# Kernel optimization log

Hardware: AMD Instinct MI355X
Metric: run time of the kernel (lower is better)

The kernel has to match this reference:

```python
import jax, jax.numpy as jnp
import numpy as np

BN_EPS = 1e-5


def setup_inputs() -> dict:
    key = jax.random.key(0)
    ks = jax.random.split(key, 8)
    B, C, H, W = 8, 256, 48, 48
    s = 1.0 / np.sqrt(C)
    x = jax.random.normal(ks[0], (B, C, H, W), dtype=jnp.float32)
    Wk = jax.random.normal(ks[1], (C, C), dtype=jnp.float32) * s
    Wq = jax.random.normal(ks[2], (C, C), dtype=jnp.float32) * s
    Wv = jax.random.normal(ks[3], (C, C), dtype=jnp.float32) * s
    W2 = jax.random.normal(ks[4], (C, C), dtype=jnp.float32) * s
    b2 = jax.random.normal(ks[5], (C,), dtype=jnp.float32) * 0.02
    gamma = jnp.ones((C,), dtype=jnp.float32)
    beta = jnp.zeros((C,), dtype=jnp.float32)
    return {"x": x, "Wk": Wk, "Wq": Wq, "Wv": Wv, "W2": W2, "b2": b2,
            "gamma": gamma, "beta": beta}


def reference(x, Wk, Wq, Wv, W2, b2, gamma, beta):
    B, C, H, W = x.shape
    N = H * W
    xf = x.reshape(B, C, N)
    # 1x1 convs == channel mixing matmuls
    k = jnp.einsum('oc,bcn->bon', Wk, xf)  # (B,C,N)
    q = jnp.einsum('oc,bcn->bon', Wq, xf)  # (B,C,N)
    v = jnp.einsum('oc,bcn->bon', Wv, xf)  # (B,C,N)
    # scores[b,n,m] = sum_c k[b,c,n] * q[b,c,m]  (unscaled, as in source)
    scores = jnp.einsum('bcn,bcm->bnm', k, q)          # (B,N,N)
    prob = jax.nn.softmax(scores, axis=2)
    # out[b,c,n] = sum_m prob[b,n,m] * v[b,c,m]
    attn = jnp.einsum('bnm,bcm->bcn', prob, v).reshape(B, C, H, W)
    # react2: 1x1 conv (with bias) + BatchNorm2d (training-mode batch stats)
    y = jnp.einsum('oc,bchw->bohw', W2, attn) + b2[None, :, None, None]
    mean = jnp.mean(y, axis=(0, 2, 3))
    var = jnp.var(y, axis=(0, 2, 3))  # biased, matches torch BN normalization
    yhat = (y - mean[None, :, None, None]) * jax.lax.rsqrt(var + BN_EPS)[None, :, None, None]
    return yhat * gamma[None, :, None, None] + beta[None, :, None, None]
```

## Files before the change

kernel.cpp:

```cpp
#include <hip/hip_runtime.h>
#include <hip/hip_fp16.h>
#include <math.h>

#define BN_EPS 1e-5f

typedef unsigned short ushort_t;
typedef unsigned int uint_t;

constexpr int BB   = 8;
constexpr int CC   = 256;
constexpr int NN   = 2304;
constexpr int MTOT = BB * NN;
constexpr int NSPLIT = 4;
constexpr int MT32 = 72;
constexpr int TPS  = 18;
constexpr int TILE = 8192;
constexpr float MFIX = 64.0f;
constexpr size_t SZE = (size_t)BB * NN * CC;

typedef short bf16x8 __attribute__((ext_vector_type(8)));
typedef _Float16 f16x8 __attribute__((ext_vector_type(8)));
typedef float f32x16 __attribute__((ext_vector_type(16)));

union F4 { float4 v; float f[4]; };
union US4 { ushort_t u[4]; uint2 v; };
union U4H8 { uint4 v; ushort_t h[8]; };

__device__ __forceinline__ ushort_t f2bf(float f) {
  uint_t u = __float_as_uint(f);
  uint_t r = u + 0x7FFFu + ((u >> 16) & 1u);
  return (ushort_t)(r >> 16);
}
__device__ __forceinline__ float bf2f(ushort_t h) {
  return __uint_as_float(((uint_t)h) << 16);
}
__device__ __forceinline__ ushort_t f2h(float f) {
  return __half_as_ushort(__float2half(f));
}
__device__ __forceinline__ uint_t pk_trunc(float lo, float hi) {
  return __builtin_amdgcn_perm(__float_as_uint(hi), __float_as_uint(lo), 0x07060302u);
}
__device__ __forceinline__ int rowmap(int reg, int laneHi) {
  return (reg & 3) + 8 * (reg >> 2) + 4 * laneHi;
}

__global__ __launch_bounds__(256) void xpose(
    const float* __restrict__ x, ushort_t* __restrict__ xh, ushort_t* __restrict__ xl)
{
  const int b = blockIdx.z, n0 = blockIdx.y * 64, c0 = blockIdx.x * 64;
  __shared__ float t_s[64][67];
  const int tid = threadIdx.x;
#pragma unroll
  for (int t = 0; t < 4; ++t) {
    int e4 = tid + t * 256;
    int r = e4 >> 4, c4 = e4 & 15;
    F4 v; v.v = *(const float4*)&x[((size_t)b * CC + c0 + r) * NN + n0 + c4 * 4];
#pragma unroll
    for (int k = 0; k < 4; ++k) t_s[r][c4 * 4 + k] = v.f[k];
  }
  __syncthreads();
#pragma unroll
  for (int t = 0; t < 4; ++t) {
    int e = tid + t * 256;
    int nr = e >> 4, cc = e & 15;
    US4 hv, lv;
#pragma unroll
    for (int k = 0; k < 4; ++k) {
      const float v = t_s[cc * 4 + k][nr];
      const ushort_t h = f2bf(v);
      hv.u[k] = h;
      lv.u[k] = f2bf(v - bf2f(h));
    }
    const size_t o = ((size_t)b * NN + n0 + nr) * CC + c0 + cc * 4;
    *(uint2*)&xh[o] = hv.v;
    *(uint2*)&xl[o] = lv.v;
  }
}

__global__ __launch_bounds__(256) void wsplit(
    const float* __restrict__ Wk, const float* __restrict__ Wq,
    const float* __restrict__ Wv, const float* __restrict__ W2,
    ushort_t* __restrict__ wh, ushort_t* __restrict__ wl,
    float* __restrict__ stats)
{
  if (blockIdx.x < 2) stats[blockIdx.x * 256 + threadIdx.x] = 0.f;
  const int mat = blockIdx.x >> 5;
  const int off = ((blockIdx.x & 31) * 256 + threadIdx.x) * 8;
  const float* Wm = (mat == 0) ? Wk : (mat == 1) ? Wq : (mat == 2) ? Wv : W2;
  F4 a, c;
  a.v = *(const float4*)&Wm[off];
  c.v = *(const float4*)&Wm[off + 4];
  U4H8 hv, lv;
#pragma unroll
  for (int j = 0; j < 8; ++j) {
    const float v = (j < 4) ? a.f[j] : c.f[j - 4];
    const ushort_t h = f2bf(v);
    hv.h[j] = h;
    lv.h[j] = f2bf(v - bf2f(h));
  }
  *(uint4*)&wh[mat * 65536 + off] = hv.v;
  *(uint4*)&wl[mat * 65536 + off] = lv.v;
}

__global__ __launch_bounds__(256, 3) void qkv_mfma(
    const ushort_t* __restrict__ xh, const ushort_t* __restrict__ xl,
    const ushort_t* __restrict__ wh, const ushort_t* __restrict__ wl,
    ushort_t* __restrict__ kf, ushort_t* __restrict__ qf,
    ushort_t* __restrict__ vt2)
{
  const int mb  = blockIdx.x;
  const int mat = blockIdx.y >> 1;
  const int nh  = blockIdx.y & 1;
  const int b   = blockIdx.z;
  const int tid = threadIdx.x, w = tid >> 6, lane = tid & 63;
  const int l31 = lane & 31, lH = lane >> 5;
  const int wm = w & 1, wn = w >> 1;

  __shared__ alignas(16) ushort_t smem[24576];

  const size_t xrow = ((size_t)b * NN + mb * 64 + lane) * CC;
  const int obase = nh * 128;
  const size_t wrow = (size_t)(obase + lane) * CC;
  const ushort_t* whm = wh + mat * 65536;
  const ushort_t* wlm = wl + mat * 65536;

  f32x16 accA[2], accB[2], accC[2];
#pragma unroll
  for (int i = 0; i < 2; ++i) {
    accA[i] = (f32x16){}; accB[i] = (f32x16){}; accC[i] = (f32x16){};
  }

#define STAGE(k0)                                                                   \
  {                                                                                 \
    _Pragma("unroll")                                                               \
    for (int cc = 0; cc < 2; ++cc) {                                                \
      const int ch = 2 * w + cc;                                                    \
      const size_t gx = xrow + (k0) + ch * 8;                                       \
      __builtin_amdgcn_global_load_lds(                                             \
          (const __attribute__((address_space(1))) uint_t*)(xh + gx),               \
          (__attribute__((address_space(3))) uint_t*)(smem + ch * 512), 16, 0, 0);  \
      __builtin_amdgcn_global_load_lds(                                             \
          (const __attribute__((address_space(1))) uint_t*)(xl + gx),               \
          (__attribute__((address_space(3))) uint_t*)(smem + 4096 + ch * 512),      \
          16, 0, 0);                                                                \
      _Pragma("unroll")                                                             \
      for (int h = 0; h < 2; ++h) {                                                 \
        const size_t gw = wrow + (size_t)h * 64 * CC + (k0) + ch * 8;               \
        __builtin_amdgcn_global_load_lds(                                           \
            (const __attribute__((address_space(1))) uint_t*)(whm + gw),            \
            (__attribute__((address_space(3))) uint_t*)(smem + 8192 + ch * 1024 +   \
                                                        h * 512), 16, 0, 0);        \
        __builtin_amdgcn_global_load_lds(                                           \
            (const __attribute__((address_space(1))) uint_t*)(wlm + gw),            \
            (__attribute__((address_space(3))) uint_t*)(smem + 16384 + ch * 1024 +  \
                                                        h * 512), 16, 0, 0);        \
      }                                                                             \
    }                                                                               \
  }

#pragma unroll
  for (int t = 0; t < 4; ++t) {
    if (t) __syncthreads();
    STAGE(t * 64)
    __syncthreads();
#pragma unroll
    for (int kc = 0; kc < 4; ++kc) {
      const int ch = kc * 2 + lH;
      const bf16x8 Ah = *(const bf16x8*)&smem[(ch * 64 + wm * 32 + l31) * 8];
      const bf16x8 Al = *(const bf16x8*)&smem[4096 + (ch * 64 + wm * 32 + l31) * 8];
#pragma unroll
      for (int ot = 0; ot < 2; ++ot) {
        const int oL = wn * 64 + ot * 32 + l31;
        const bf16x8 Bh = *(const bf16x8*)&smem[8192 + (ch * 128 + oL) * 8];
        const bf16x8 Bl = *(const bf16x8*)&smem[16384 + (ch * 128 + oL) * 8];
        accA[ot] = __builtin_amdgcn_mfma_f32_32x32x16_bf16(Ah, Bh, accA[ot], 0, 0, 0);
        accB[ot] = __builtin_amdgcn_mfma_f32_32x32x16_bf16(Ah, Bl, accB[ot], 0, 0, 0);
        accC[ot] = __builtin_amdgcn_mfma_f32_32x32x16_bf16(Al, Bh, accC[ot], 0, 0, 0);
      }
    }
  }
#undef STAGE
  __syncthreads();

  ushort_t* vscr = smem + w * 1280;
  const int mt = mb * 2 + wm;
  const size_t tbase = (size_t)(b * MT32 + mt) * TILE;
#pragma unroll
  for (int ot = 0; ot < 2; ++ot) {
    const int o0 = obase + wn * 64 + ot * 32;
    if (mat < 2) {
#pragma unroll
      for (int reg = 0; reg < 16; ++reg)
        vscr[rowmap(reg, lH) * 40 + l31] =
            f2h(accA[ot][reg] + accB[ot][reg] + accC[ot][reg]);
      ushort_t* ob = ((mat == 0) ? kf : qf) + tbase;
#pragma unroll
      for (int k2 = 0; k2 < 2; ++k2) {
        const int idx = k2 * 64 + lane;
        const int n = idx >> 2, coct = idx & 3;
        uint4 pk = *(const uint4*)&vscr[n * 40 + coct * 8];
        *(uint4*)&ob[(size_t)(((o0 >> 3) + coct) * 32 + n) * 8] = pk;
      }
    } else {
#pragma unroll
      for (int reg = 0; reg < 16; ++reg)
        vscr[l31 * 40 + rowmap(reg, lH)] =
            f2bf(accA[ot][reg] + accB[ot][reg] + accC[ot][reg]);
#pragma unroll
      for (int k2 = 0; k2 < 2; ++k2) {
        const int idx = k2 * 64 + lane;
        const int cl = idx >> 2, moct = idx & 3;
        uint4 pk = *(const uint4*)&vscr[cl * 40 + moct * 8];
        *(uint4*)&vt2[tbase + (size_t)(moct * 256 + o0 + cl) * 8] = pk;
      }
    }
  }
}

__global__ __launch_bounds__(256, 2) void attn_fused(
    const ushort_t* __restrict__ kf, const ushort_t* __restrict__ qf,
    const ushort_t* __restrict__ vt2,
    ushort_t* __restrict__ Opart, float* __restrict__ Ls)
{
  const int id = blockIdx.x + 18 * (blockIdx.y + 4 * blockIdx.z);
  const int xcd = id & 7, s = id >> 3;
  const int g = xcd * 4 + s / 18;
  const int n0 = (s % 18) * 128;
  const int split = g & 3, b = g >> 2;

  const int tid = threadIdx.x;
  const int w = tid >> 6, lane = tid & 63;
  const int l31 = lane & 31, lH = lane >> 5;

  __shared__ alignas(16) ushort_t sQ[2 * TILE];
  __shared__ alignas(16) ushort_t sV[2 * TILE];
  __shared__ alignas(16) ushort_t sPt[4 * 1280];
  ushort_t* Pt = sPt + w * 1280;

  const ushort_t* qtb = qf + (size_t)(b * MT32 + split * TPS) * TILE;
  const ushort_t* vtb = vt2 + (size_t)(b * MT32 + split * TPS) * TILE;

  f16x8 Kf[16];
  {
    const ushort_t* kt = kf + (size_t)(b * MT32 + (n0 >> 5) + w) * TILE;
#pragma unroll
    for (int kc = 0; kc < 16; ++kc)
      Kf[kc] = *(const f16x8*)&kt[(size_t)((kc * 2 + lH) * 32 + l31) * 8];
  }
  f32x16 O[8];
#pragma unroll
  for (int i = 0; i < 8; ++i) O[i] = (f32x16){};
  float rsum = 0.f;

#define ISSUE_TILE(tt, buf)                                                        \
  {                                                                                \
    const ushort_t* qs = qtb + (size_t)(tt) * TILE;                                \
    const ushort_t* vs = vtb + (size_t)(tt) * TILE;                                \
    ushort_t* ldq = sQ + (buf) * TILE;                                             \
    ushort_t* ldv = sV + (buf) * TILE;                                             \
    _Pragma("unroll")                                                              \
    for (int j = 0; j < 4; ++j) {                                                  \
      const int i = w * 4 + j;                                                     \
      __builtin_amdgcn_global_load_lds(                                            \
          (const __attribute__((address_space(1))) uint_t*)(qs + i * 512 + lane * 8), \
          (__attribute__((address_space(3))) uint_t*)(ldq + i * 512), 16, 0, 0);   \
      __builtin_amdgcn_global_load_lds(                                            \
          (const __attribute__((address_space(1))) uint_t*)(vs + i * 512 + lane * 8), \
          (__attribute__((address_space(3))) uint_t*)(ldv + i * 512), 16, 0, 0);   \
    }                                                                              \
  }

  ISSUE_TILE(0, 0)
  ISSUE_TILE(1, 1)
  __syncthreads();

  for (int t = 0; t < TPS; ++t) {
    const int cur = t & 1;
    const ushort_t* Qs = sQ + cur * TILE;
    const ushort_t* Vs = sV + cur * TILE;
    f32x16 acc = {};
#pragma unroll
    for (int kc = 0; kc < 16; ++kc) {
      f16x8 Aq = *(const f16x8*)&Qs[(size_t)((kc * 2 + lH) * 32 + l31) * 8];
      acc = __builtin_amdgcn_mfma_f32_32x32x16_f16(Aq, Kf[kc], acc, 0, 0, 0);
    }
#pragma unroll
    for (int j = 0; j < 4; ++j) {
      float p0 = __expf(acc[4 * j]     - MFIX);
      float p1 = __expf(acc[4 * j + 1] - MFIX);
      float p2 = __expf(acc[4 * j + 2] - MFIX);
      float p3 = __expf(acc[4 * j + 3] - MFIX);
      rsum += (p0 + p1) + (p2 + p3);
      uint2 pk;
      pk.x = pk_trunc(p0, p1);
      pk.y = pk_trunc(p2, p3);
      *(uint2*)&Pt[l31 * 40 + 8 * j + 4 * lH] = pk;
    }
#pragma unroll
    for (int ks = 0; ks < 2; ++ks) {
      bf16x8 Bp = *(const bf16x8*)&Pt[l31 * 40 + ks * 16 + lH * 8];
#pragma unroll
      for (int cg = 0; cg < 8; ++cg) {
        bf16x8 Av = *(const bf16x8*)&Vs[(size_t)((ks * 2 + lH) * 256 + cg * 32 + l31) * 8];
        O[cg] = __builtin_amdgcn_mfma_f32_32x32x16_bf16(Av, Bp, O[cg], 0, 0, 0);
      }
    }
    __syncthreads();
    if (t + 2 < TPS) ISSUE_TILE(t + 2, cur)
  }
#undef ISSUE_TILE

  ushort_t* Ob = Opart + (size_t)(split * BB + b) * CC * NN;
  const int n = n0 + w * 32 + l31;
#pragma unroll
  for (int cg = 0; cg < 8; ++cg)
#pragma unroll
    for (int reg = 0; reg < 16; ++reg) {
      const int c = cg * 32 + rowmap(reg, lH);
      Ob[(size_t)c * NN + n] = f2bf(O[cg][reg]);
    }
  rsum += __shfl_xor(rsum, 32);
  if (lH == 0)
    Ls[(size_t)split * MTOT + b * NN + n] = rsum;
}

__global__ __launch_bounds__(256, 2) void proj_f(
    const ushort_t* __restrict__ Opart, const float* __restrict__ Ls,
    const ushort_t* __restrict__ w2h, const ushort_t* __restrict__ w2l,
    const float* __restrict__ b2,
    ushort_t* __restrict__ yb, float* __restrict__ stats)
{
  const int mt = blockIdx.x;
  const int tid = threadIdx.x, w = tid >> 6, lane = tid & 63;
  const int l31 = lane & 31, lH = lane >> 5, h8 = lH * 8;
  const int r0 = mt * 32;
  const int b = r0 / NN, nb = r0 % NN;

  __shared__ alignas(16) ushort_t t_s[32 * 264];
  __shared__ float inv_s[32];

  if (tid < 32) {
    float L = 0.f;
#pragma unroll
    for (int sp = 0; sp < NSPLIT; ++sp) L += Ls[(size_t)sp * MTOT + r0 + tid];
    inv_s[tid] = 1.0f / L;
  }
  __syncthreads();

  const size_t obase = ((size_t)b * CC) * NN + nb;
#pragma unroll
  for (int k = 0; k < 4; ++k) {
    const int c = (tid >> 2) + k * 64;
    const int noct = tid & 3;
    float accv[8] = {};
#pragma unroll
    for (int sp = 0; sp < NSPLIT; ++sp) {
      U4H8 pk;
      pk.v = *(const uint4*)&Opart[(size_t)sp * SZE + obase + (size_t)c * NN + noct * 8];
#pragma unroll
      for (int j = 0; j < 8; ++j) accv[j] += bf2f(pk.h[j]);
    }
#pragma unroll
    for (int j = 0; j < 8; ++j) {
      const int nl = noct * 8 + j;
      t_s[nl * 264 + c] = f2bf(accv[j] * inv_s[nl]);
    }
  }
  __syncthreads();

  bf16x8 Af[16];
#pragma unroll
  for (int kc = 0; kc < 16; ++kc)
    Af[kc] = *(const bf16x8*)&t_s[l31 * 264 + kc * 16 + h8];

#pragma unroll
  for (int ot = 0; ot < 2; ++ot) {
    const int o0 = w * 64 + ot * 32;
    f32x16 accA = {}, accB = {};
#pragma unroll
    for (int kc = 0; kc < 16; ++kc) {
      bf16x8 Bh = *(const bf16x8*)&w2h[(size_t)(o0 + l31) * CC + kc * 16 + h8];
      bf16x8 Bl = *(const bf16x8*)&w2l[(size_t)(o0 + l31) * CC + kc * 16 + h8];
      accA = __builtin_amdgcn_mfma_f32_32x32x16_bf16(Af[kc], Bh, accA, 0, 0, 0);
      accB = __builtin_amdgcn_mfma_f32_32x32x16_bf16(Af[kc], Bl, accB, 0, 0, 0);
    }
    const float bj = b2[o0 + l31];
    float cs = 0.f, cq = 0.f;
#pragma unroll
    for (int reg = 0; reg < 16; ++reg) {
      const float v = accA[reg] + accB[reg] + bj;
      yb[(size_t)(r0 + rowmap(reg, lH)) * CC + o0 + l31] = f2bf(v);
      cs += v;
      cq += v * v;
    }
    cs += __shfl_xor(cs, 32);
    cq += __shfl_xor(cq, 32);
    if (lane < 32) {
      atomicAdd(&stats[o0 + l31], cs);
      atomicAdd(&stats[CC + o0 + l31], cq);
    }
  }
}

__global__ __launch_bounds__(256) void bn_out(
    const ushort_t* __restrict__ yb, const float* __restrict__ stats,
    const float* __restrict__ gamma, const float* __restrict__ beta,
    float* __restrict__ out)
{
  const int b = blockIdx.z, n0 = blockIdx.y * 64, c0 = blockIdx.x * 64;
  __shared__ alignas(16) ushort_t t_s[64 * 72];
  __shared__ float aa[64], bbf[64];
  const int tid = threadIdx.x;
  if (tid < 64) {
    const int c = c0 + tid;
    const float mean = stats[c] * (1.0f / MTOT);
    const float var  = stats[CC + c] * (1.0f / MTOT) - mean * mean;
    const float rstd = rsqrtf(var + BN_EPS);
    const float a = rstd * gamma[c];
    aa[tid]  = a;
    bbf[tid] = beta[c] - mean * a;
  }
#pragma unroll
  for (int t = 0; t < 2; ++t) {
    const int e = tid + t * 256;
    const int r = e >> 3, c8 = e & 7;
    const int sc8 = c8 ^ (r & 7);
    *(uint4*)&t_s[r * 72 + sc8 * 8] =
        *(const uint4*)&yb[((size_t)b * NN + n0 + r) * CC + c0 + c8 * 8];
  }
  __syncthreads();
#pragma unroll
  for (int t = 0; t < 4; ++t) {
    const int e4 = tid + t * 256;
    const int cr = e4 >> 4, r4 = e4 & 15;
    const float a = aa[cr], bb2 = bbf[cr];
    F4 o4;
#pragma unroll
    for (int k = 0; k < 4; ++k) {
      const int r = r4 * 4 + k;
      const int idx = r * 72 + (((cr >> 3) ^ (r & 7)) << 3) + (cr & 7);
      o4.f[k] = bf2f(t_s[idx]) * a + bb2;
    }
    *(float4*)&out[((size_t)b * CC + c0 + cr) * NN + n0 + r4 * 4] = o4.v;
  }
}

extern "C" void kernel_launch(void* const* d_in, const int* in_sizes, int n_in,
                              void* d_out, int out_size, void* d_ws, size_t ws_size,
                              hipStream_t stream)
{
  (void)in_sizes; (void)n_in; (void)out_size; (void)ws_size;
  const float* x     = (const float*)d_in[0];
  const float* Wk    = (const float*)d_in[1];
  const float* Wq    = (const float*)d_in[2];
  const float* Wv    = (const float*)d_in[3];
  const float* W2    = (const float*)d_in[4];
  const float* b2    = (const float*)d_in[5];
  const float* gamma = (const float*)d_in[6];
  const float* beta  = (const float*)d_in[7];
  float* out = (float*)d_out;

  ushort_t* u   = (ushort_t*)d_ws;
  ushort_t* xh  = u;
  ushort_t* xl  = u + SZE;
  ushort_t* kf  = u + 2 * SZE;
  ushort_t* qf  = u + 3 * SZE;
  ushort_t* vt2 = u + 4 * SZE;
  ushort_t* Opart = u + 5 * SZE;
  ushort_t* wh  = u + (5 + NSPLIT) * SZE;
  ushort_t* wl  = wh + 4 * 65536;
  float* Ls    = (float*)(wl + 4 * 65536);
  float* stats = Ls + (size_t)NSPLIT * MTOT;
  ushort_t* yb = u;

  xpose     <<<dim3(4, 36, 8),       256, 0, stream>>>(x, xh, xl);
  wsplit    <<<dim3(128),            256, 0, stream>>>(Wk, Wq, Wv, W2, wh, wl, stats);
  qkv_mfma  <<<dim3(36, 6, 8),       256, 0, stream>>>(xh, xl, wh, wl, kf, qf, vt2);
  attn_fused<<<dim3(18, NSPLIT, 8),  256, 0, stream>>>(kf, qf, vt2, Opart, Ls);
  proj_f    <<<dim3(576),            256, 0, stream>>>(Opart, Ls, wh + 3 * 65536,
                                                       wl + 3 * 65536, b2, yb, stats);
  bn_out    <<<dim3(4, 36, 8),       256, 0, stream>>>(yb, stats, gamma, beta, out);
}
```

Before: 247.1 us.

## Stage W2 through LDS with async loads and raise MFMA wave priority

The attention kernel now raises wave priority with s_setprio around its MFMA bursts, so matrix instructions get issued ahead of other waves' work. The projection kernel no longer reads W2 hi/lo fragments straight from global memory per lane. It stages W2 in 32-column chunks into LDS with global_load_lds, keeping accumulators for both output tiles live across chunks, and raises its occupancy target to 3 blocks per CU. This adds barriers per chunk and more register and LDS pressure in exchange for coalesced weight loads.

```diff
diff --git a/kernel.cpp b/kernel.cpp
--- a/kernel.cpp
+++ b/kernel.cpp
@@ -279,11 +279,13 @@
     const ushort_t* Qs = sQ + cur * TILE;
     const ushort_t* Vs = sV + cur * TILE;
     f32x16 acc = {};
+    __builtin_amdgcn_s_setprio(1);
 #pragma unroll
     for (int kc = 0; kc < 16; ++kc) {
       f16x8 Aq = *(const f16x8*)&Qs[(size_t)((kc * 2 + lH) * 32 + l31) * 8];
       acc = __builtin_amdgcn_mfma_f32_32x32x16_f16(Aq, Kf[kc], acc, 0, 0, 0);
     }
+    __builtin_amdgcn_s_setprio(0);
 #pragma unroll
     for (int j = 0; j < 4; ++j) {
       float p0 = __expf(acc[4 * j]     - MFIX);
@@ -299,11 +301,13 @@
 #pragma unroll
     for (int ks = 0; ks < 2; ++ks) {
       bf16x8 Bp = *(const bf16x8*)&Pt[l31 * 40 + ks * 16 + lH * 8];
+      __builtin_amdgcn_s_setprio(1);
 #pragma unroll
       for (int cg = 0; cg < 8; ++cg) {
         bf16x8 Av = *(const bf16x8*)&Vs[(size_t)((ks * 2 + lH) * 256 + cg * 32 + l31) * 8];
         O[cg] = __builtin_amdgcn_mfma_f32_32x32x16_bf16(Av, Bp, O[cg], 0, 0, 0);
       }
+      __builtin_amdgcn_s_setprio(0);
     }
     __syncthreads();
     if (t + 2 < TPS) ISSUE_TILE(t + 2, cur)
@@ -324,7 +328,7 @@
     Ls[(size_t)split * MTOT + b * NN + n] = rsum;
 }
 
-__global__ __launch_bounds__(256, 2) void proj_f(
+__global__ __launch_bounds__(256, 3) void proj_f(
     const ushort_t* __restrict__ Opart, const float* __restrict__ Ls,
     const ushort_t* __restrict__ w2h, const ushort_t* __restrict__ w2l,
     const float* __restrict__ b2,
@@ -337,6 +341,7 @@
   const int b = r0 / NN, nb = r0 % NN;
 
   __shared__ alignas(16) ushort_t t_s[32 * 264];
+  __shared__ alignas(16) ushort_t sW[16384];
   __shared__ float inv_s[32];
 
   if (tid < 32) {
@@ -373,22 +378,47 @@
   for (int kc = 0; kc < 16; ++kc)
     Af[kc] = *(const bf16x8*)&t_s[l31 * 264 + kc * 16 + h8];
 
+  f32x16 accA[2], accB[2];
+#pragma unroll
+  for (int i = 0; i < 2; ++i) { accA[i] = (f32x16){}; accB[i] = (f32x16){}; }
+
+  const size_t wbase = (size_t)(w * 64 + lane) * CC;
+
+  for (int ch = 0; ch < 8; ++ch) {
+    if (ch) __syncthreads();
+#pragma unroll
+    for (int j = 0; j < 8; ++j) {
+      const int hl = j >> 2, k4 = j & 3;
+      const ushort_t* src = (hl ? w2l : w2h) + wbase + ch * 32 + k4 * 8;
+      __builtin_amdgcn_global_load_lds(
+          (const __attribute__((address_space(1))) uint_t*)src,
+          (__attribute__((address_space(3))) uint_t*)(sW + ((hl * 4 + k4) * 256 + w * 64) * 8),
+          16, 0, 0);
+    }
+    __syncthreads();
+#pragma unroll
+    for (int kl = 0; kl < 2; ++kl) {
+      const int kc = ch * 2 + kl;
+      const int ks = kl * 2 + lH;
+#pragma unroll
+      for (int ot = 0; ot < 2; ++ot) {
+        const int oL = w * 64 + ot * 32 + l31;
+        const bf16x8 Bh = *(const bf16x8*)&sW[(size_t)(ks * 256 + oL) * 8];
+        const bf16x8 Bl = *(const bf16x8*)&sW[(size_t)((4 + ks) * 256 + oL) * 8];
+        accA[ot] = __builtin_amdgcn_mfma_f32_32x32x16_bf16(Af[kc], Bh, accA[ot], 0, 0, 0);
+        accB[ot] = __builtin_amdgcn_mfma_f32_32x32x16_bf16(Af[kc], Bl, accB[ot], 0, 0, 0);
+      }
+    }
+  }
+
 #pragma unroll
   for (int ot = 0; ot < 2; ++ot) {
     const int o0 = w * 64 + ot * 32;
-    f32x16 accA = {}, accB = {};
-#pragma unroll
-    for (int kc = 0; kc < 16; ++kc) {
-      bf16x8 Bh = *(const bf16x8*)&w2h[(size_t)(o0 + l31) * CC + kc * 16 + h8];
-      bf16x8 Bl = *(const bf16x8*)&w2l[(size_t)(o0 + l31) * CC + kc * 16 + h8];
-      accA = __builtin_amdgcn_mfma_f32_32x32x16_bf16(Af[kc], Bh, accA, 0, 0, 0);
-      accB = __builtin_amdgcn_mfma_f32_32x32x16_bf16(Af[kc], Bl, accB, 0, 0, 0);
-    }
     const float bj = b2[o0 + l31];
     float cs = 0.f, cq = 0.f;
 #pragma unroll
     for (int reg = 0; reg < 16; ++reg) {
-      const float v = accA[reg] + accB[reg] + bj;
+      const float v = accA[ot][reg] + accB[ot][reg] + bj;
       yb[(size_t)(r0 + rowmap(reg, lH)) * CC + o0 + l31] = f2bf(v);
       cs += v;
       cq += v * v;
```

Measured after the change: 253.4 us. 1.03x slower.
